# Performance work log

Measured on AMD Instinct MI355X. Metric: run time of the kernel, lower is better.

Reference implementation:

```python
import jax, jax.numpy as jnp
import numpy as np

HID = 768
PATCH = 32
IMG = 384
PD = IMG // PATCH          # 12
NPATCH = PD * PD           # 144
MAXLEN = 144               # config.max_image_length (== num_patches)
VOCAB = 30522
SEQ = 40
B = 64
EPS = 1e-12


def _layernorm(x, g, b):
    mu = jnp.mean(x, axis=-1, keepdims=True)
    var = jnp.mean(jnp.square(x - mu), axis=-1, keepdims=True)
    return (x - mu) / jnp.sqrt(var + EPS) * g + b


def _bilinear_pad(sp, h, w, out_h, out_w):
    # sp: [C, PD, PD]; bilinear (align_corners=True) resize to (h, w), zero-pad to (out_h, out_w)
    pd = sp.shape[1]
    hf = jnp.maximum(h - 1, 1).astype(jnp.float32)
    wf = jnp.maximum(w - 1, 1).astype(jnp.float32)
    ry = jnp.arange(out_h, dtype=jnp.float32) * (pd - 1) / hf
    rx = jnp.arange(out_w, dtype=jnp.float32) * (pd - 1) / wf
    y0 = jnp.clip(jnp.floor(ry).astype(jnp.int32), 0, pd - 1)
    x0 = jnp.clip(jnp.floor(rx).astype(jnp.int32), 0, pd - 1)
    y1 = jnp.minimum(y0 + 1, pd - 1)
    x1 = jnp.minimum(x0 + 1, pd - 1)
    wy = (ry - y0.astype(jnp.float32))[:, None]   # [out_h,1]
    wx = (rx - x0.astype(jnp.float32))[None, :]   # [1,out_w]
    a = sp[:, y0][:, :, x0]
    b = sp[:, y0][:, :, x1]
    c = sp[:, y1][:, :, x0]
    d = sp[:, y1][:, :, x1]
    val = a * (1 - wy) * (1 - wx) + b * (1 - wy) * wx + c * wy * (1 - wx) + d * wy * wx
    valid = (jnp.arange(out_h)[:, None] < h) & (jnp.arange(out_w)[None, :] < w)
    return val * valid  # [C,out_h,out_w]


def setup_inputs():
    key = jax.random.key(0)
    ks = jax.random.split(key, 12)
    s = 0.02
    return {
        "input_ids": jax.random.randint(ks[0], (B, SEQ), 0, VOCAB, dtype=jnp.int32),
        "attention_mask": jnp.ones((B, SEQ), dtype=jnp.int32),
        "token_type_ids": jnp.zeros((B, SEQ), dtype=jnp.int32),
        "pixel_values": jax.random.normal(ks[1], (B, 3, IMG, IMG), jnp.float32),
        "pixel_mask": jnp.ones((B, IMG, IMG), dtype=jnp.int32),
        "word_emb": jax.random.normal(ks[2], (VOCAB, HID), jnp.float32) * s,
        "pos_emb_text": jax.random.normal(ks[3], (SEQ, HID), jnp.float32) * s,
        "tok_type_emb": jax.random.normal(ks[4], (2, HID), jnp.float32) * s,
        "ln_gamma": jnp.ones((HID,), jnp.float32),
        "ln_beta": jnp.zeros((HID,), jnp.float32),
        "cls_token": jax.random.normal(ks[5], (1, 1, HID), jnp.float32) * s,
        "conv_w": jax.random.normal(ks[6], (HID, 3, PATCH, PATCH), jnp.float32) * s,
        "conv_b": jnp.zeros((HID,), jnp.float32),
        "vis_pos_emb": jax.random.normal(ks[7], (1, NPATCH + 1, HID), jnp.float32) * s,
        "modality_emb": jax.random.normal(ks[8], (2, HID), jnp.float32) * s,
        "image_token_type_idx": 1,
    }


def reference(input_ids, attention_mask, token_type_ids, pixel_values, pixel_mask,
              word_emb, pos_emb_text, tok_type_emb, ln_gamma, ln_beta, cls_token,
              conv_w, conv_b, vis_pos_emb, modality_emb, image_token_type_idx):
    bsz, seq = input_ids.shape

    # ---- text embeddings ----
    te = word_emb[input_ids] + tok_type_emb[token_type_ids] + pos_emb_text[None, :seq]
    te = _layernorm(te, ln_gamma, ln_beta)

    # ---- patch conv projection ----
    x = jax.lax.conv_general_dilated(
        pixel_values, conv_w, (PATCH, PATCH), 'VALID',
        dimension_numbers=('NCHW', 'OIHW', 'NCHW')) + conv_b[None, :, None, None]
    _, C, H, W = x.shape

    # ---- nearest-downsample pixel mask to patch grid ----
    iy = (jnp.arange(H) * (pixel_mask.shape[1] // H))
    ix = (jnp.arange(W) * (pixel_mask.shape[2] // W))
    xm = pixel_mask[:, iy][:, :, ix]          # [B,H,W] int
    x_h = xm.sum(axis=1)[:, 0]                # valid rows per image
    x_w = xm.sum(axis=2)[:, 0]                # valid cols per image

    # ---- per-sample bilinear interp of spatial position embeddings ----
    sp = vis_pos_emb[0, 1:].T.reshape(C, PD, PD)
    pos = jax.vmap(lambda h, w: _bilinear_pad(sp, h, w, H, W))(x_h, x_w)  # [B,C,H,W]

    # ---- deterministic gather: valid patches first (original order), then invalid pads ----
    N = H * W
    mask_flat = xm.reshape(bsz, N)
    keys = (1 - mask_flat) * (N + 1) + jnp.arange(N)[None, :]
    sel = jnp.argsort(keys, axis=1)[:, :MAXLEN]                 # [B,L]

    x_tok = jnp.take_along_axis(x.reshape(bsz, C, N).transpose(0, 2, 1), sel[:, :, None], axis=1)
    pos_tok = jnp.take_along_axis(pos.reshape(bsz, C, N).transpose(0, 2, 1), sel[:, :, None], axis=1)
    m_tok = jnp.take_along_axis(mask_flat, sel, axis=1)

    cls = jnp.broadcast_to(cls_token, (bsz, 1, C))
    pos_cls = jnp.broadcast_to(vis_pos_emb[:, :1], (bsz, 1, C))
    x_img = jnp.concatenate([cls, x_tok], axis=1) + jnp.concatenate([pos_cls, pos_tok], axis=1)
    m_img = jnp.concatenate([jnp.ones((bsz, 1), m_tok.dtype), m_tok], axis=1)

    # ---- modality (token-type) embeddings ----
    te = te + modality_emb[0][None, None, :]
    x_img = x_img + modality_emb[image_token_type_idx][None, None, :]

    embeddings = jnp.concatenate([te, x_img], axis=1)           # [B, seq+1+L, HID]
    masks = jnp.concatenate([attention_mask.astype(jnp.int32), m_img.astype(jnp.int32)], axis=1)
    return embeddings, masks
```

## Files before the change

### kernel.cpp

```cpp
#include <hip/hip_runtime.h>
#include <hip/hip_bf16.h>
#include <stdint.h>

typedef __hip_bfloat16 bf16;
typedef __bf16 bf16x8 __attribute__((ext_vector_type(8)));
typedef float f32x4 __attribute__((ext_vector_type(4)));
typedef unsigned short u16x8 __attribute__((ext_vector_type(8)));

#define HID   768
#define SEQL  40
#define TOK   185
#define NP    144
#define PD2   12
#define KDIM  3072
#define IMGSZ 384
#define IMG2  147456

#define WSB_PIX 0
#define WSB_W   56623104
#define WSB_INT 61341696
#define WS_DST 0
#define WS_SRC 9216
#define WS_MV  18432
#define WS_XH  27648
#define WS_XW  27712

#define EMB_ELEMS (64 * TOK * HID)

#define NB_PIXC 2048
#define NB_WC   128
#define NB_TEXT (64 * SEQL)
#define BID_WC   NB_PIXC
#define BID_TEXT (NB_PIXC + NB_WC)
#define BID_PREP (BID_TEXT + NB_TEXT)
#define BID_CLS  (BID_PREP + 64)
#define NB_TOTAL (BID_CLS + 64)

#define N8_PIX (28311552 / 8)
#define N8_W   (2359296 / 8)

__device__ __forceinline__ unsigned short f2bu(float x) {
    uint32_t u = __float_as_uint(x);
    return (unsigned short)((u + 0x7FFFu + ((u >> 16) & 1u)) >> 16);
}

__global__ __launch_bounds__(256) void pre_kernel(
    const float* __restrict__ pixf, unsigned short* __restrict__ pixb,
    const float* __restrict__ Wc, unsigned short* __restrict__ wb,
    const int* __restrict__ ids, const int* __restrict__ tts,
    const float* __restrict__ wemb, const float* __restrict__ ptext,
    const float* __restrict__ ttemb, const float* __restrict__ g,
    const float* __restrict__ be, const float* __restrict__ modal,
    const int* __restrict__ pmask, const float* __restrict__ cls,
    const float* __restrict__ vpos, const int* __restrict__ tti,
    const int* __restrict__ attn, int* __restrict__ ws,
    float* __restrict__ out) {
    int bid = blockIdx.x, tid = threadIdx.x;
    if (bid < NB_PIXC) {
        for (int i = bid * 256 + tid; i < N8_PIX; i += NB_PIXC * 256) {
            f32x4 a = ((const f32x4*)pixf)[2 * i];
            f32x4 b = ((const f32x4*)pixf)[2 * i + 1];
            u16x8 r;
#pragma unroll
            for (int j = 0; j < 4; j++) r[j] = f2bu(a[j]);
#pragma unroll
            for (int j = 0; j < 4; j++) r[4 + j] = f2bu(b[j]);
            ((u16x8*)pixb)[i] = r;
        }
    } else if (bid < BID_TEXT) {
        for (int i = (bid - BID_WC) * 256 + tid; i < N8_W; i += NB_WC * 256) {
            f32x4 a = ((const f32x4*)Wc)[2 * i];
            f32x4 b = ((const f32x4*)Wc)[2 * i + 1];
            u16x8 r;
#pragma unroll
            for (int j = 0; j < 4; j++) r[j] = f2bu(a[j]);
#pragma unroll
            for (int j = 0; j < 4; j++) r[4 + j] = f2bu(b[j]);
            ((u16x8*)wb)[i] = r;
        }
    } else if (bid < BID_PREP) {
        int blk = bid - BID_TEXT;
        int b = blk / SEQL, s = blk % SEQL;
        int id = ids[b * SEQL + s];
        int tt = tts[b * SEQL + s];
        const float* wr = wemb + (size_t)id * HID;
        const float* tr = ttemb + (size_t)tt * HID;
        const float* pr = ptext + s * HID;
        float x[3], s1 = 0.f, s2 = 0.f;
#pragma unroll
        for (int k = 0; k < 3; k++) {
            int n = tid + k * 256;
            float xv = wr[n] + tr[n] + pr[n];
            x[k] = xv; s1 += xv; s2 += xv * xv;
        }
        for (int off = 32; off; off >>= 1) {
            s1 += __shfl_down(s1, off);
            s2 += __shfl_down(s2, off);
        }
        __shared__ float red[8];
        int lane = tid & 63, wid = tid >> 6;
        if (lane == 0) { red[wid] = s1; red[4 + wid] = s2; }
        __syncthreads();
        float ts1 = red[0] + red[1] + red[2] + red[3];
        float ts2 = red[4] + red[5] + red[6] + red[7];
        float mu = ts1 * (1.0f / HID);
        float var = ts2 * (1.0f / HID) - mu * mu;
        float rstd = rsqrtf(var + 1e-12f);
        float* orow = out + ((size_t)(b * TOK + s)) * HID;
#pragma unroll
        for (int k = 0; k < 3; k++) {
            int n = tid + k * 256;
            orow[n] = (x[k] - mu) * rstd * g[n] + be[n] + modal[n];
        }
    } else if (bid < BID_CLS) {
        int b = bid - BID_PREP;
        __shared__ int v[NP];
        if (tid < NP) {
            int i = tid / PD2, j = tid % PD2;
            v[tid] = pmask[(size_t)b * IMG2 + (size_t)(i * 32) * IMGSZ + (j * 32)];
        }
        __syncthreads();
        if (tid == 0) {
            int nv = 0;
            for (int p = 0; p < NP; p++) nv += (v[p] != 0);
            int cv = 0, ci = 0;
            for (int p = 0; p < NP; p++) {
                int d = v[p] ? (cv++) : (nv + ci++);
                ws[WS_DST + b * NP + p] = d;
                ws[WS_SRC + b * NP + d] = p;
                ws[WS_MV + b * NP + p] = v[p];
            }
            int h = 0, w = 0;
            for (int i = 0; i < PD2; i++) h += v[i * PD2];
            for (int j = 0; j < PD2; j++) w += v[j];
            ws[WS_XH + b] = h;
            ws[WS_XW + b] = w;
        }
    } else {
        int b = bid - BID_CLS;
        int tt = *tti;
        const float* modalr = modal + tt * HID;
        float* orow = out + ((size_t)(b * TOK + SEQL)) * HID;
#pragma unroll
        for (int k = 0; k < 3; k++) {
            int n = tid + k * 256;
            orow[n] = cls[n] + vpos[n] + modalr[n];
        }
        __shared__ int v2[NP];
        if (tid < NP) {
            int i = tid / PD2, j = tid % PD2;
            v2[tid] = pmask[(size_t)b * IMG2 + (size_t)(i * 32) * IMGSZ + (j * 32)];
        }
        __syncthreads();
        __shared__ int srcl[NP];
        if (tid == 0) {
            int nv = 0;
            for (int p = 0; p < NP; p++) nv += (v2[p] != 0);
            int cv = 0, ci = 0;
            for (int p = 0; p < NP; p++) {
                int d = v2[p] ? (cv++) : (nv + ci++);
                srcl[d] = p;
            }
        }
        __syncthreads();
        float* om = out + (size_t)EMB_ELEMS + (size_t)b * TOK;
        if (tid < TOK) {
            float mv;
            if (tid < SEQL) mv = (float)attn[b * SEQL + tid];
            else if (tid == SEQL) mv = 1.0f;
            else mv = (float)v2[srcl[tid - (SEQL + 1)]];
            om[tid] = mv;
        }
    }
}

__global__ __launch_bounds__(256, 2) void gemm_kernel(
    const bf16* __restrict__ pix, const bf16* __restrict__ W,
    const float* __restrict__ bias, const float* __restrict__ vpos,
    const float* __restrict__ modal, const int* __restrict__ tti,
    const int* __restrict__ ws, float* __restrict__ out) {
    __shared__ unsigned short As[2 * 128 * 64];
    __shared__ unsigned short Bs[2 * 128 * 64];

    int bid = blockIdx.x;
    int swz = (bid & 7) * 54 + (bid >> 3);
    int bm = swz / 6, bn = swz - bm * 6;
    int m0 = bm << 7, n0 = bn << 7;

    int tid = threadIdx.x;
    int lane = tid & 63, wid = tid >> 6;
    int wm = wid >> 1, wn = wid & 1;

    int kof = (tid & 7) << 3;
    size_t apix[4]; size_t wbase[4]; int kofs[4];
#pragma unroll
    for (int r = 0; r < 4; r++) {
        int row = (tid >> 3) + r * 32;
        kofs[r] = kof ^ ((row & 7) << 3);
        int gm = m0 + row;
        int b_ = gm / NP; int p_ = gm - b_ * NP;
        int ii = p_ / PD2, jj = p_ - ii * PD2;
        apix[r] = (size_t)(b_ * 3) * IMG2 + (size_t)(ii * 32) * IMGSZ + (jj * 32);
        wbase[r] = (size_t)(n0 + row) * KDIM + kofs[r];
    }

    f32x4 acc[4][4];
#pragma unroll
    for (int a = 0; a < 4; a++)
#pragma unroll
        for (int c = 0; c < 4; c++) acc[a][c] = (f32x4){0.f, 0.f, 0.f, 0.f};

#define STAGE(BUF, KT)                                                              \
    {                                                                               \
        _Pragma("unroll")                                                           \
        for (int r = 0; r < 4; r++) {                                               \
            int k = (KT) + kofs[r];                                                 \
            int ci = k >> 10; int rem = k & 1023;                                   \
            size_t cioff = (size_t)ci * IMG2 + (size_t)(rem >> 5) * IMGSZ + (rem & 31); \
            const bf16* ga = pix + apix[r] + cioff;                                 \
            const bf16* gb = W + wbase[r] + (KT);                                   \
            unsigned short* la = As + (BUF) * 8192 + r * 2048 + wid * 512;          \
            unsigned short* lb = Bs + (BUF) * 8192 + r * 2048 + wid * 512;          \
            __builtin_amdgcn_global_load_lds(                                       \
                (const __attribute__((address_space(1))) unsigned int*)ga,          \
                (__attribute__((address_space(3))) unsigned int*)la, 16, 0, 0);     \
            __builtin_amdgcn_global_load_lds(                                       \
                (const __attribute__((address_space(1))) unsigned int*)gb,          \
                (__attribute__((address_space(3))) unsigned int*)lb, 16, 0, 0);     \
        }                                                                           \
    }

#define COMPUTE(BUF)                                                                \
    {                                                                               \
        _Pragma("unroll")                                                           \
        for (int ks = 0; ks < 2; ks++) {                                            \
            int kb = (ks << 5) + ((lane >> 4) << 3);                                \
            bf16x8 af[4], bfr[4];                                                   \
            _Pragma("unroll")                                                       \
            for (int mi = 0; mi < 4; mi++) {                                        \
                int row = (wm << 6) + (mi << 4) + (lane & 15);                      \
                af[mi] = *(const bf16x8*)&As[(BUF) * 8192 + row * 64 + (kb ^ ((row & 7) << 3))]; \
            }                                                                       \
            _Pragma("unroll")                                                       \
            for (int nj = 0; nj < 4; nj++) {                                        \
                int row = (wn << 6) + (nj << 4) + (lane & 15);                      \
                bfr[nj] = *(const bf16x8*)&Bs[(BUF) * 8192 + row * 64 + (kb ^ ((row & 7) << 3))]; \
            }                                                                       \
            __builtin_amdgcn_s_setprio(1);                                          \
            _Pragma("unroll")                                                       \
            for (int mi = 0; mi < 4; mi++)                                          \
                _Pragma("unroll")                                                   \
                for (int nj = 0; nj < 4; nj++)                                      \
                    acc[mi][nj] = __builtin_amdgcn_mfma_f32_16x16x32_bf16(          \
                        af[mi], bfr[nj], acc[mi][nj], 0, 0, 0);                     \
            __builtin_amdgcn_s_setprio(0);                                          \
        }                                                                           \
    }

    STAGE(0, 0);
    for (int kt = 0; kt < KDIM; kt += 64) {
        int buf = (kt >> 6) & 1;
        __syncthreads();
        if (kt + 64 < KDIM) STAGE(buf ^ 1, kt + 64);
        COMPUTE(buf);
    }
#undef STAGE
#undef COMPUTE

    int tt = *tti;
    const float* modalr = modal + tt * HID;
    int r16 = lane >> 4, c16 = lane & 15;
#pragma unroll
    for (int mi = 0; mi < 4; mi++) {
#pragma unroll
        for (int reg = 0; reg < 4; reg++) {
            int gm = m0 + (wm << 6) + (mi << 4) + (r16 << 2) + reg;
            int b_ = gm / NP; int p_ = gm - b_ * NP;
            int ii = p_ / PD2, jj = p_ - ii * PD2;
            int h = ws[WS_XH + b_], w = ws[WS_XW + b_];
            float hf = (float)((h - 1) > 1 ? (h - 1) : 1);
            float wf = (float)((w - 1) > 1 ? (w - 1) : 1);
            float ry = (float)(ii * (PD2 - 1)) / hf;
            float rx = (float)(jj * (PD2 - 1)) / wf;
            int y0 = (int)floorf(ry); y0 = y0 < 0 ? 0 : (y0 > PD2 - 1 ? PD2 - 1 : y0);
            int x0 = (int)floorf(rx); x0 = x0 < 0 ? 0 : (x0 > PD2 - 1 ? PD2 - 1 : x0);
            int y1 = y0 + 1 > PD2 - 1 ? PD2 - 1 : y0 + 1;
            int x1 = x0 + 1 > PD2 - 1 ? PD2 - 1 : x0 + 1;
            float wy = ry - (float)y0, wx = rx - (float)x0;
            float vs = ((ii < h) && (jj < w)) ? 1.0f : 0.0f;
            float w00 = (1.f - wy) * (1.f - wx) * vs, w01 = (1.f - wy) * wx * vs;
            float w10 = wy * (1.f - wx) * vs, w11 = wy * wx * vs;
            const float* p00 = vpos + (size_t)(1 + y0 * PD2 + x0) * HID;
            const float* p01 = vpos + (size_t)(1 + y0 * PD2 + x1) * HID;
            const float* p10 = vpos + (size_t)(1 + y1 * PD2 + x0) * HID;
            const float* p11 = vpos + (size_t)(1 + y1 * PD2 + x1) * HID;
            int drow = ws[WS_DST + b_ * NP + p_];
            float* orow = out + ((size_t)(b_ * TOK + SEQL + 1 + drow)) * HID;
#pragma unroll
            for (int nj = 0; nj < 4; nj++) {
                int n = n0 + (wn << 6) + (nj << 4) + c16;
                float pos = w00 * p00[n] + w01 * p01[n] + w10 * p10[n] + w11 * p11[n];
                orow[n] = acc[mi][nj][reg] + bias[n] + pos + modalr[n];
            }
        }
    }
}

extern "C" void kernel_launch(void* const* d_in, const int* in_sizes, int n_in,
                              void* d_out, int out_size, void* d_ws, size_t ws_size,
                              hipStream_t stream) {
    const int* ids = (const int*)d_in[0];
    const int* attn = (const int*)d_in[1];
    const int* tts = (const int*)d_in[2];
    const float* pix = (const float*)d_in[3];
    const int* pmask = (const int*)d_in[4];
    const float* wemb = (const float*)d_in[5];
    const float* ptext = (const float*)d_in[6];
    const float* ttemb = (const float*)d_in[7];
    const float* g = (const float*)d_in[8];
    const float* be = (const float*)d_in[9];
    const float* cls = (const float*)d_in[10];
    const float* Wc = (const float*)d_in[11];
    const float* bias = (const float*)d_in[12];
    const float* vpos = (const float*)d_in[13];
    const float* modal = (const float*)d_in[14];
    const int* tti = (const int*)d_in[15];
    float* out = (float*)d_out;

    unsigned short* pixb = (unsigned short*)((char*)d_ws + WSB_PIX);
    unsigned short* wb = (unsigned short*)((char*)d_ws + WSB_W);
    int* wsi = (int*)((char*)d_ws + WSB_INT);

    pre_kernel<<<NB_TOTAL, 256, 0, stream>>>(pix, pixb, Wc, wb, ids, tts, wemb, ptext,
                                             ttemb, g, be, modal, pmask, cls, vpos, tti,
                                             attn, wsi, out);
    gemm_kernel<<<432, 256, 0, stream>>>((const bf16*)pixb, (const bf16*)wb,
                                         bias, vpos, modal, tti, wsi, out);
}
```

Baseline: 104.3 us.

## Use 4-stage BK=32 LDS pipeline with explicit vmcnt waits in patch GEMM

Replaces the double-buffered 64-wide K tile with a four-buffer 32-wide K ring. Loads are issued three stages ahead and synchronised through explicit s_waitcnt vmcnt plus raw barriers instead of __syncthreads, so several tiles of global-to-LDS traffic stay in flight. LDS offsets and the XOR swizzle are precomputed per lane for the narrower tile, removing address arithmetic from the inner loop. The cost is more barriers per K element and reliance on exact vmcnt counting, which is fragile if the compiler reorders the memory operations.

```diff
diff --git a/kernel.cpp b/kernel.cpp
--- a/kernel.cpp
+++ b/kernel.cpp
@@ -179,8 +179,8 @@
     const float* __restrict__ bias, const float* __restrict__ vpos,
     const float* __restrict__ modal, const int* __restrict__ tti,
     const int* __restrict__ ws, float* __restrict__ out) {
-    __shared__ unsigned short As[2 * 128 * 64];
-    __shared__ unsigned short Bs[2 * 128 * 64];
+    __shared__ unsigned short As[4 * 128 * 32];
+    __shared__ unsigned short Bs[4 * 128 * 32];
 
     int bid = blockIdx.x;
     int swz = (bid & 7) * 54 + (bid >> 3);
@@ -191,36 +191,52 @@
     int lane = tid & 63, wid = tid >> 6;
     int wm = wid >> 1, wn = wid & 1;
 
-    int kof = (tid & 7) << 3;
-    size_t apix[4]; size_t wbase[4]; int kofs[4];
-#pragma unroll
-    for (int r = 0; r < 4; r++) {
-        int row = (tid >> 3) + r * 32;
-        kofs[r] = kof ^ ((row & 7) << 3);
+    int c = tid & 3;
+    size_t apix[2]; size_t wbase[2]; int kof8[2];
+#pragma unroll
+    for (int r = 0; r < 2; r++) {
+        int row = (tid >> 2) + r * 64;
+        int m_ = (row ^ (row >> 2)) & 3;
+        kof8[r] = (c ^ m_) << 3;
         int gm = m0 + row;
         int b_ = gm / NP; int p_ = gm - b_ * NP;
         int ii = p_ / PD2, jj = p_ - ii * PD2;
         apix[r] = (size_t)(b_ * 3) * IMG2 + (size_t)(ii * 32) * IMGSZ + (jj * 32);
-        wbase[r] = (size_t)(n0 + row) * KDIM + kofs[r];
+        wbase[r] = (size_t)(n0 + row) * KDIM + kof8[r];
+    }
+
+    int j16 = lane >> 4;
+    int aoff[4], boff[4];
+#pragma unroll
+    for (int mi = 0; mi < 4; mi++) {
+        int row = (wm << 6) + (mi << 4) + (lane & 15);
+        int m_ = (row ^ (row >> 2)) & 3;
+        aoff[mi] = row * 64 + ((j16 ^ m_) << 4);
+    }
+#pragma unroll
+    for (int nj = 0; nj < 4; nj++) {
+        int row = (wn << 6) + (nj << 4) + (lane & 15);
+        int m_ = (row ^ (row >> 2)) & 3;
+        boff[nj] = row * 64 + ((j16 ^ m_) << 4);
     }
 
     f32x4 acc[4][4];
 #pragma unroll
     for (int a = 0; a < 4; a++)
 #pragma unroll
-        for (int c = 0; c < 4; c++) acc[a][c] = (f32x4){0.f, 0.f, 0.f, 0.f};
+        for (int cc = 0; cc < 4; cc++) acc[a][cc] = (f32x4){0.f, 0.f, 0.f, 0.f};
 
 #define STAGE(BUF, KT)                                                              \
     {                                                                               \
         _Pragma("unroll")                                                           \
-        for (int r = 0; r < 4; r++) {                                               \
-            int k = (KT) + kofs[r];                                                 \
+        for (int r = 0; r < 2; r++) {                                               \
+            int k = (KT) + kof8[r];                                                 \
             int ci = k >> 10; int rem = k & 1023;                                   \
             size_t cioff = (size_t)ci * IMG2 + (size_t)(rem >> 5) * IMGSZ + (rem & 31); \
             const bf16* ga = pix + apix[r] + cioff;                                 \
             const bf16* gb = W + wbase[r] + (KT);                                   \
-            unsigned short* la = As + (BUF) * 8192 + r * 2048 + wid * 512;          \
-            unsigned short* lb = Bs + (BUF) * 8192 + r * 2048 + wid * 512;          \
+            unsigned short* la = As + (BUF) * 4096 + r * 2048 + wid * 512;          \
+            unsigned short* lb = Bs + (BUF) * 4096 + r * 2048 + wid * 512;          \
             __builtin_amdgcn_global_load_lds(                                       \
                 (const __attribute__((address_space(1))) unsigned int*)ga,          \
                 (__attribute__((address_space(3))) unsigned int*)la, 16, 0, 0);     \
@@ -230,40 +246,43 @@
         }                                                                           \
     }
 
-#define COMPUTE(BUF)                                                                \
+#define COMPUTE(BUFBYTE)                                                            \
     {                                                                               \
+        bf16x8 af[4], bfr[4];                                                       \
         _Pragma("unroll")                                                           \
-        for (int ks = 0; ks < 2; ks++) {                                            \
-            int kb = (ks << 5) + ((lane >> 4) << 3);                                \
-            bf16x8 af[4], bfr[4];                                                   \
+        for (int mi = 0; mi < 4; mi++)                                              \
+            af[mi] = *(const bf16x8*)((const char*)As + (BUFBYTE) + aoff[mi]);      \
+        _Pragma("unroll")                                                           \
+        for (int nj = 0; nj < 4; nj++)                                              \
+            bfr[nj] = *(const bf16x8*)((const char*)Bs + (BUFBYTE) + boff[nj]);     \
+        __builtin_amdgcn_s_setprio(1);                                              \
+        _Pragma("unroll")                                                           \
+        for (int mi = 0; mi < 4; mi++)                                              \
             _Pragma("unroll")                                                       \
-            for (int mi = 0; mi < 4; mi++) {                                        \
-                int row = (wm << 6) + (mi << 4) + (lane & 15);                      \
-                af[mi] = *(const bf16x8*)&As[(BUF) * 8192 + row * 64 + (kb ^ ((row & 7) << 3))]; \
-            }                                                                       \
-            _Pragma("unroll")                                                       \
-            for (int nj = 0; nj < 4; nj++) {                                        \
-                int row = (wn << 6) + (nj << 4) + (lane & 15);                      \
-                bfr[nj] = *(const bf16x8*)&Bs[(BUF) * 8192 + row * 64 + (kb ^ ((row & 7) << 3))]; \
-            }                                                                       \
-            __builtin_amdgcn_s_setprio(1);                                          \
-            _Pragma("unroll")                                                       \
-            for (int mi = 0; mi < 4; mi++)                                          \
-                _Pragma("unroll")                                                   \
-                for (int nj = 0; nj < 4; nj++)                                      \
-                    acc[mi][nj] = __builtin_amdgcn_mfma_f32_16x16x32_bf16(          \
-                        af[mi], bfr[nj], acc[mi][nj], 0, 0, 0);                     \
-            __builtin_amdgcn_s_setprio(0);                                          \
-        }                                                                           \
+            for (int nj = 0; nj < 4; nj++)                                          \
+                acc[mi][nj] = __builtin_amdgcn_mfma_f32_16x16x32_bf16(              \
+                    af[mi], bfr[nj], acc[mi][nj], 0, 0, 0);                         \
+        __builtin_amdgcn_s_setprio(0);                                              \
     }
 
     STAGE(0, 0);
-    for (int kt = 0; kt < KDIM; kt += 64) {
-        int buf = (kt >> 6) & 1;
-        __syncthreads();
-        if (kt + 64 < KDIM) STAGE(buf ^ 1, kt + 64);
-        COMPUTE(buf);
-    }
+    STAGE(1, 32);
+    STAGE(2, 64);
+    for (int s = 0; s < 94; ++s) {
+        asm volatile("s_waitcnt vmcnt(8)" ::: "memory");
+        __builtin_amdgcn_s_barrier();
+        __builtin_amdgcn_sched_barrier(0);
+        if (s < 93) STAGE((s + 3) & 3, (s + 3) << 5);
+        COMPUTE((s & 3) * 8192);
+    }
+    asm volatile("s_waitcnt vmcnt(4)" ::: "memory");
+    __builtin_amdgcn_s_barrier();
+    __builtin_amdgcn_sched_barrier(0);
+    COMPUTE(2 * 8192);
+    asm volatile("s_waitcnt vmcnt(0)" ::: "memory");
+    __builtin_amdgcn_s_barrier();
+    __builtin_amdgcn_sched_barrier(0);
+    COMPUTE(3 * 8192);
 #undef STAGE
 #undef COMPUTE
 
```

Result: slower. 122.5 us (+17.5%).
